# Performance work log

Measured on AMD Instinct MI355X. Metric: run time of the kernel, lower is better.

## Reference

```python
import jax, jax.numpy as jnp
import numpy as np

R, B, N, I, O, NB = 8, 4, 1024, 64, 64, 4
EPS = 1e-7  # keras.backend.epsilon()


def setup_inputs() -> dict:
    key = jax.random.key(0)
    ks = jax.random.split(key, 6)
    features = jax.random.normal(ks[0], (B, N, I), jnp.float32)
    adj = jax.random.randint(ks[1], (R, B, N, N), 0, 2, jnp.int32)  # stacked A[i]
    weight = jax.random.normal(ks[2], (NB, I, O), jnp.float32) * 0.1  # basis weights
    Wo = jax.random.normal(ks[3], (I, O), jnp.float32) * 0.1          # self-loop weight
    w_cmp = jax.random.normal(ks[4], (R, NB), jnp.float32) * 0.1      # basis coefficients
    b = jax.random.normal(ks[5], (O,), jnp.float32) * 0.1             # bias
    return {"features": features, "adj": adj, "weight": weight, "Wo": Wo, "w_cmp": w_cmp, "b": b}


def reference(features, adj, weight, Wo, w_cmp, b):
    # basis decomposition: per-relation weight [R, I, O]
    w_full = jnp.einsum('rb,bio->rio', w_cmp, weight)
    adj_f = adj.astype(features.dtype)                      # [R, B, N, N]
    # per-relation transform: x_r = features @ W_r -> [R, B, N, O]
    x = jnp.einsum('bni,rio->rbno', features, w_full)
    # batch_dot(edges^T, x): agg[r,b,n] = sum_m edges[r,b,m,n] * x[r,b,m]
    agg = jnp.einsum('rbmn,rbmo->rbno', adj_f, x)
    # original normalizer: K.sum(edges, axis=2, keepdims=True) -> row sums over last axis
    deg = adj_f.sum(axis=-1, keepdims=True)                 # [R, B, N, 1]
    agg = agg / (deg + EPS)
    self_x = features @ Wo                                  # [B, N, O]
    # concatenate [x_0 | x_1 | ... | x_{R-1} | self] along features
    concat = jnp.concatenate(
        [agg.transpose(1, 2, 0, 3).reshape(B, N, R * O), self_x], axis=-1
    )                                                       # [B, N, (R+1)*O]
    # faithful to original: reshape (..., O, R+1) then sum last axis
    out = concat.reshape(-1, N, O, R + 1).sum(axis=-1)      # [B, N, O]
    out = out + b
    return jax.nn.relu(out)
```

## Files before the change

### kernel.cpp

```cpp
#include <hip/hip_runtime.h>
#include <hip/hip_bf16.h>


#define NN 1024
#define EPSK 1e-7f

typedef __bf16 bf16x8 __attribute__((ext_vector_type(8)));
typedef float f32x4 __attribute__((ext_vector_type(4)));

__device__ __forceinline__ unsigned short f2bf(float f) {
  union { float f; unsigned int u; } v; v.f = f;
  return (unsigned short)((v.u + 0x7FFFu + ((v.u >> 16) & 1u)) >> 16);
}

__global__ __launch_bounds__(256) void prep_kernel(
    const float* __restrict__ feat,
    const float* __restrict__ weight,
    const float* __restrict__ Wo,
    const float* __restrict__ wcmp,
    float* __restrict__ xf,
    float* __restrict__ selfP,
    float* __restrict__ deg)
{
  __shared__ __align__(16) unsigned short featL[128 * 72];
  __shared__ __align__(16) float wTf[64 * 65];
  __shared__ __align__(16) unsigned short wfold[16 * 72];
  __shared__ __align__(16) float stg[128 * 8];

  const int bid = blockIdx.x;
  const int t = threadIdx.x;
  const bool isSelf = bid >= 256;
  int r, b, chunk;
  if (!isSelf) { r = bid >> 5; b = (bid >> 3) & 3; chunk = bid & 7; }
  else { const int s2 = bid - 256; b = s2 >> 3; chunk = s2 & 7; r = 8; }
  const int n0 = chunk << 7;

  if (bid < 32) {
    for (int k = t; k < NN; k += 256) deg[bid * NN + k] = 0.0f;
  }

  const float* fsrc = feat + ((size_t)(b * NN + n0)) * 64;
  #pragma unroll
  for (int p = 0; p < 8; ++p) {
    const int idx = p * 256 + t;
    const int row = idx >> 4, c4 = idx & 15;
    const float4 v = *reinterpret_cast<const float4*>(fsrc + row * 64 + c4 * 4);
    ushort4 u;
    u.x = f2bf(v.x); u.y = f2bf(v.y); u.z = f2bf(v.z); u.w = f2bf(v.w);
    *reinterpret_cast<ushort4*>(&featL[row * 72 + c4 * 4]) = u;
  }

  if (!isSelf) {
    const float wc0 = wcmp[r * 4 + 0], wc1 = wcmp[r * 4 + 1];
    const float wc2 = wcmp[r * 4 + 2], wc3 = wcmp[r * 4 + 3];
    #pragma unroll
    for (int jj = 0; jj < 16; ++jj) {
      const int e = jj * 256 + t;
      const int i = e >> 6, c = e & 63;
      wTf[c * 65 + i] = wc0 * weight[i * 64 + c] + wc1 * weight[4096 + i * 64 + c] +
                        wc2 * weight[8192 + i * 64 + c] + wc3 * weight[12288 + i * 64 + c];
    }
  } else {
    #pragma unroll
    for (int jj = 0; jj < 16; ++jj) {
      const int e = jj * 256 + t;
      const int i = e >> 6, c = e & 63;
      wTf[c * 65 + i] = Wo[i * 64 + c];
    }
  }
  __syncthreads();

  #pragma unroll
  for (int jj = 0; jj < 4; ++jj) {
    const int e = jj * 256 + t;
    const int s = e >> 6, i = e & 63;
    float sum = 0.f;
    if (s < 8) {
      const int c0 = 9 * s - r;
      const int clo = c0 < 0 ? 0 : c0;
      const int chi = (c0 + 8 > 63) ? 63 : c0 + 8;
      for (int c = clo; c <= chi; ++c) sum += wTf[c * 65 + i];
    }
    wfold[s * 72 + i] = f2bf(sum);
  }
  __syncthreads();

  const int w = t >> 6, lane = t & 63;
  const int li = lane & 15, lg = lane >> 4;

  f32x4 acc0 = {0.f, 0.f, 0.f, 0.f}, acc1 = {0.f, 0.f, 0.f, 0.f};
  #pragma unroll
  for (int ks = 0; ks < 2; ++ks) {
    const int kof = ks * 32 + lg * 8;
    const bf16x8 af = __builtin_bit_cast(bf16x8,
        *reinterpret_cast<const uint4*>(&wfold[li * 72 + kof]));
    const bf16x8 b0 = __builtin_bit_cast(bf16x8,
        *reinterpret_cast<const uint4*>(&featL[((2 * w + 0) * 16 + li) * 72 + kof]));
    const bf16x8 b1 = __builtin_bit_cast(bf16x8,
        *reinterpret_cast<const uint4*>(&featL[((2 * w + 1) * 16 + li) * 72 + kof]));
    acc0 = __builtin_amdgcn_mfma_f32_16x16x32_bf16(af, b0, acc0, 0, 0, 0);
    acc1 = __builtin_amdgcn_mfma_f32_16x16x32_bf16(af, b1, acc1, 0, 0, 0);
  }

  if (lg < 2) {
    #pragma unroll
    for (int qq = 0; qq < 4; ++qq) {
      const int s = lg * 4 + qq;
      stg[((2 * w + 0) * 16 + li) * 8 + s] = acc0[qq];
      stg[((2 * w + 1) * 16 + li) * 8 + s] = acc1[qq];
    }
  }
  __syncthreads();
  {
    float* dstF = isSelf ? (selfP + ((size_t)(b * NN + n0)) * 8)
                         : (xf + ((size_t)((r * 4 + b) * NN + n0)) * 8);
    *reinterpret_cast<float4*>(dstF + t * 4) =
        *reinterpret_cast<const float4*>(&stg[t * 4]);
  }
}

__global__ __launch_bounds__(256) void agg_kernel(
    const int* __restrict__ adj,
    const float* __restrict__ xf,
    float* __restrict__ aggP,
    float* __restrict__ deg)
{
  __shared__ __align__(16) float xsL[256 * 8];
  __shared__ __align__(16) float degL[256 * 66];

  const int bid = blockIdx.x;
  const int rb = bid >> 4, mq = (bid >> 2) & 3, nq = bid & 3;
  const int t = threadIdx.x;
  const int tm = t >> 6, tn = t & 63;
  const int mbase = mq << 8, nbase = nq << 8;

  {
    const float* xs = xf + ((size_t)(rb * NN + mbase)) * 8;
    *reinterpret_cast<float4*>(&xsL[t * 8]) = *reinterpret_cast<const float4*>(xs + t * 8);
    *reinterpret_cast<float4*>(&xsL[t * 8 + 4]) = *reinterpret_cast<const float4*>(xs + t * 8 + 4);
  }

  const int* asrc = adj + (((size_t)rb) << 20) + ((size_t)mbase << 10) + nbase + (tn << 2);

  float acc[4][8];
  #pragma unroll
  for (int j = 0; j < 4; ++j)
    #pragma unroll
    for (int s = 0; s < 8; ++s) acc[j][s] = 0.f;

  __syncthreads();

  int4 buf0 = *reinterpret_cast<const int4*>(asrc + ((size_t)(0 * 4 + tm) << 10));
  int4 buf1 = *reinterpret_cast<const int4*>(asrc + ((size_t)(1 * 4 + tm) << 10));
  int4 buf2 = *reinterpret_cast<const int4*>(asrc + ((size_t)(2 * 4 + tm) << 10));
  int4 buf3 = *reinterpret_cast<const int4*>(asrc + ((size_t)(3 * 4 + tm) << 10));

#define AGG_BODY(BUF, I)                                                        \
  {                                                                             \
    const int4 cur_ = BUF;                                                      \
    const int ml_ = ((I) << 2) + tm;                                            \
    if ((I) < 60) {                                                             \
      BUF = *reinterpret_cast<const int4*>(asrc + ((size_t)(ml_ + 16) << 10));  \
    }                                                                           \
    const float a0_ = (float)cur_.x, a1_ = (float)cur_.y;                       \
    const float a2_ = (float)cur_.z, a3_ = (float)cur_.w;                       \
    degL[ml_ * 66 + tn] = (float)(cur_.x + cur_.y + cur_.z + cur_.w);           \
    const float4 xlo_ = *reinterpret_cast<const float4*>(&xsL[ml_ * 8]);        \
    const float4 xhi_ = *reinterpret_cast<const float4*>(&xsL[ml_ * 8 + 4]);    \
    const float xs_[8] = {xlo_.x, xlo_.y, xlo_.z, xlo_.w,                       \
                          xhi_.x, xhi_.y, xhi_.z, xhi_.w};                      \
    _Pragma("unroll")                                                           \
    for (int s_ = 0; s_ < 8; ++s_) {                                            \
      acc[0][s_] = fmaf(a0_, xs_[s_], acc[0][s_]);                              \
      acc[1][s_] = fmaf(a1_, xs_[s_], acc[1][s_]);                              \
      acc[2][s_] = fmaf(a2_, xs_[s_], acc[2][s_]);                              \
      acc[3][s_] = fmaf(a3_, xs_[s_], acc[3][s_]);                              \
    }                                                                           \
  }

  for (int ib = 0; ib < 16; ++ib) {
    AGG_BODY(buf0, ib * 4 + 0);
    AGG_BODY(buf1, ib * 4 + 1);
    AGG_BODY(buf2, ib * 4 + 2);
    AGG_BODY(buf3, ib * 4 + 3);
  }
#undef AGG_BODY

  __syncthreads();

  {
    float s = 0.f;
    #pragma unroll
    for (int k = 0; k < 32; ++k) {
      const float2 v = *reinterpret_cast<const float2*>(&degL[t * 66 + 2 * k]);
      s += v.x + v.y;
    }
    atomicAdd(&deg[rb * NN + mbase + t], s);
  }
  __syncthreads();

  float* accL = degL;
  #pragma unroll
  for (int j = 0; j < 4; ++j) {
    *reinterpret_cast<float4*>(&accL[t * 36 + j * 8]) =
        make_float4(acc[j][0], acc[j][1], acc[j][2], acc[j][3]);
    *reinterpret_cast<float4*>(&accL[t * 36 + j * 8 + 4]) =
        make_float4(acc[j][4], acc[j][5], acc[j][6], acc[j][7]);
  }
  __syncthreads();
  {
    const int nl = t;
    const int tn2 = nl >> 2, j2 = nl & 3;
    float o8[8];
    #pragma unroll
    for (int s = 0; s < 8; ++s) o8[s] = 0.f;
    #pragma unroll
    for (int tm2 = 0; tm2 < 4; ++tm2) {
      const int base = (tm2 * 64 + tn2) * 36 + j2 * 8;
      const float4 lo = *reinterpret_cast<const float4*>(&accL[base]);
      const float4 hi = *reinterpret_cast<const float4*>(&accL[base + 4]);
      o8[0] += lo.x; o8[1] += lo.y; o8[2] += lo.z; o8[3] += lo.w;
      o8[4] += hi.x; o8[5] += hi.y; o8[6] += hi.z; o8[7] += hi.w;
    }
    float* dst = aggP + (((size_t)(mq * 32 + rb)) * NN + nbase + nl) * 8;
    *reinterpret_cast<float4*>(dst) = make_float4(o8[0], o8[1], o8[2], o8[3]);
    *reinterpret_cast<float4*>(dst + 4) = make_float4(o8[4], o8[5], o8[6], o8[7]);
  }
}

__global__ __launch_bounds__(256) void out_kernel(
    const float* __restrict__ aggP,
    const float* __restrict__ selfP,
    const float* __restrict__ deg,
    const float* __restrict__ bias, float* __restrict__ out)
{
  const int gid = blockIdx.x * 256 + threadIdx.x;
  const int o = gid & 63;
  const int n = (gid >> 6) & 1023;
  const int b = gid >> 16;

  const int r1 = (9 * o) >> 6;
  const int r2 = (9 * o + 8) >> 6;

  float acc = bias[o];
  #pragma unroll
  for (int pass = 0; pass < 2; ++pass) {
    const int r = pass ? r2 : r1;
    if (pass && r2 == r1) break;
    const int s = o - 7 * r;
    float v;
    if (r < 8) {
      const size_t base = (((size_t)(r * 4 + b)) * NN + n) * 8 + s;
      v = aggP[base] + aggP[base + 262144] + aggP[base + 524288] + aggP[base + 786432];
      v /= (deg[(r * 4 + b) * NN + n] + EPSK);
    } else {
      v = selfP[((size_t)(b * NN + n)) * 8 + (o - 56)];
    }
    acc += v;
  }
  out[gid] = fmaxf(acc, 0.0f);
}

extern "C" void kernel_launch(void* const* d_in, const int* in_sizes, int n_in,
                              void* d_out, int out_size, void* d_ws, size_t ws_size,
                              hipStream_t stream) {
  const float* feat   = (const float*)d_in[0];
  const int*   adj    = (const int*)d_in[1];
  const float* weight = (const float*)d_in[2];
  const float* Wo     = (const float*)d_in[3];
  const float* wcmp   = (const float*)d_in[4];
  const float* bias   = (const float*)d_in[5];
  float* out = (float*)d_out;

  char* ws = (char*)d_ws;
  float* xf    = (float*)(ws);
  float* selfP = (float*)(ws + 1048576u);
  float* aggP  = (float*)(ws + 1048576u + 131072u);
  float* deg   = (float*)(ws + 1048576u + 131072u + 4194304u);

  prep_kernel<<<dim3(288), dim3(256), 0, stream>>>(feat, weight, Wo, wcmp, xf, selfP, deg);
  agg_kernel<<<dim3(512), dim3(256), 0, stream>>>(adj, xf, aggP, deg);
  out_kernel<<<dim3(1024), dim3(256), 0, stream>>>(aggP, selfP, deg, bias, out);
}
```

Baseline: 35.24 us.

## Retile aggregation so each block owns full adjacency rows and computes degree directly

The aggregation kernel now gives each block 128 source rows across all 1024 destination columns, so each thread accumulates four columns over all rows without cross-warp reduction. This lets the kernel compute each row's degree completely within one block using byte-packed partial sums in shared memory, which removes the atomicAdd, the deg zeroing in the prep kernel and the shared-memory accumulator reduction. The cost is that partial aggregates are split 8 ways instead of 4, doubling the aggP workspace and the reads in the output kernel. The grid also halves to 256 blocks, each holding 16 int4 prefetches in registers under launch_bounds(256,1).

New measurement: 38.42 us. +9.0%, slower.

```diff
diff --git a/kernel.cpp b/kernel.cpp
--- a/kernel.cpp
+++ b/kernel.cpp
@@ -19,8 +19,7 @@
     const float* __restrict__ Wo,
     const float* __restrict__ wcmp,
     float* __restrict__ xf,
-    float* __restrict__ selfP,
-    float* __restrict__ deg)
+    float* __restrict__ selfP)
 {
   __shared__ __align__(16) unsigned short featL[128 * 72];
   __shared__ __align__(16) float wTf[64 * 65];
@@ -34,10 +33,6 @@
   if (!isSelf) { r = bid >> 5; b = (bid >> 3) & 3; chunk = bid & 7; }
   else { const int s2 = bid - 256; b = s2 >> 3; chunk = s2 & 7; r = 8; }
   const int n0 = chunk << 7;
-
-  if (bid < 32) {
-    for (int k = t; k < NN; k += 256) deg[bid * NN + k] = 0.0f;
-  }
 
   const float* fsrc = feat + ((size_t)(b * NN + n0)) * 64;
   #pragma unroll
@@ -119,112 +114,118 @@
   }
 }
 
-__global__ __launch_bounds__(256) void agg_kernel(
+#define BODY(PK, G, K, PF)                                                      \
+  {                                                                             \
+    const int4 cur_ = PK;                                                       \
+    if (PF) {                                                                   \
+      PK = *reinterpret_cast<const int4*>(asrc + ((((G) << 4) + (K) + 16) << 10)); \
+    }                                                                           \
+    const int ps_ = cur_.x + cur_.y + cur_.z + cur_.w;                          \
+    pk |= ((unsigned int)ps_) << (8 * ((K) & 3));                               \
+    const float a0_ = (float)cur_.x, a1_ = (float)cur_.y;                       \
+    const float a2_ = (float)cur_.z, a3_ = (float)cur_.w;                       \
+    const float4 xlo_ =                                                         \
+        *reinterpret_cast<const float4*>(&xsL[(((G) << 4) + (K)) * 8]);         \
+    const float4 xhi_ =                                                         \
+        *reinterpret_cast<const float4*>(&xsL[(((G) << 4) + (K)) * 8 + 4]);     \
+    const float xv_[8] = {xlo_.x, xlo_.y, xlo_.z, xlo_.w,                       \
+                          xhi_.x, xhi_.y, xhi_.z, xhi_.w};                      \
+    _Pragma("unroll")                                                           \
+    for (int s_ = 0; s_ < 8; ++s_) {                                            \
+      acc0[s_] = fmaf(a0_, xv_[s_], acc0[s_]);                                  \
+      acc1[s_] = fmaf(a1_, xv_[s_], acc1[s_]);                                  \
+      acc2[s_] = fmaf(a2_, xv_[s_], acc2[s_]);                                  \
+      acc3[s_] = fmaf(a3_, xv_[s_], acc3[s_]);                                  \
+    }                                                                           \
+    if (((K) & 3) == 3) {                                                       \
+      degL[((G) * 4 + ((K) >> 2)) * 260 + t] = pk;                              \
+      pk = 0u;                                                                  \
+    }                                                                           \
+  }
+
+#define GROUP(G, PF)                                                            \
+  BODY(P0, G, 0, PF) BODY(P1, G, 1, PF) BODY(P2, G, 2, PF) BODY(P3, G, 3, PF)   \
+  BODY(P4, G, 4, PF) BODY(P5, G, 5, PF) BODY(P6, G, 6, PF) BODY(P7, G, 7, PF)   \
+  BODY(P8, G, 8, PF) BODY(P9, G, 9, PF) BODY(P10, G, 10, PF)                    \
+  BODY(P11, G, 11, PF) BODY(P12, G, 12, PF) BODY(P13, G, 13, PF)                \
+  BODY(P14, G, 14, PF) BODY(P15, G, 15, PF)
+
+__global__ __launch_bounds__(256, 1) void agg_kernel(
     const int* __restrict__ adj,
     const float* __restrict__ xf,
     float* __restrict__ aggP,
     float* __restrict__ deg)
 {
-  __shared__ __align__(16) float xsL[256 * 8];
-  __shared__ __align__(16) float degL[256 * 66];
+  __shared__ __align__(16) float xsL[128 * 8];
+  __shared__ __align__(16) unsigned int degL[32 * 260];
 
   const int bid = blockIdx.x;
-  const int rb = bid >> 4, mq = (bid >> 2) & 3, nq = bid & 3;
+  const int rb = bid >> 3, mc = bid & 7;
+  const int m0 = mc << 7;
   const int t = threadIdx.x;
-  const int tm = t >> 6, tn = t & 63;
-  const int mbase = mq << 8, nbase = nq << 8;
+
+  const int* asrc = adj + (((size_t)rb) << 20) + (((size_t)m0) << 10) + (t << 2);
+
+  int4 P0  = *reinterpret_cast<const int4*>(asrc + (0 << 10));
+  int4 P1  = *reinterpret_cast<const int4*>(asrc + (1 << 10));
+  int4 P2  = *reinterpret_cast<const int4*>(asrc + (2 << 10));
+  int4 P3  = *reinterpret_cast<const int4*>(asrc + (3 << 10));
+  int4 P4  = *reinterpret_cast<const int4*>(asrc + (4 << 10));
+  int4 P5  = *reinterpret_cast<const int4*>(asrc + (5 << 10));
+  int4 P6  = *reinterpret_cast<const int4*>(asrc + (6 << 10));
+  int4 P7  = *reinterpret_cast<const int4*>(asrc + (7 << 10));
+  int4 P8  = *reinterpret_cast<const int4*>(asrc + (8 << 10));
+  int4 P9  = *reinterpret_cast<const int4*>(asrc + (9 << 10));
+  int4 P10 = *reinterpret_cast<const int4*>(asrc + (10 << 10));
+  int4 P11 = *reinterpret_cast<const int4*>(asrc + (11 << 10));
+  int4 P12 = *reinterpret_cast<const int4*>(asrc + (12 << 10));
+  int4 P13 = *reinterpret_cast<const int4*>(asrc + (13 << 10));
+  int4 P14 = *reinterpret_cast<const int4*>(asrc + (14 << 10));
+  int4 P15 = *reinterpret_cast<const int4*>(asrc + (15 << 10));
 
   {
-    const float* xs = xf + ((size_t)(rb * NN + mbase)) * 8;
-    *reinterpret_cast<float4*>(&xsL[t * 8]) = *reinterpret_cast<const float4*>(xs + t * 8);
-    *reinterpret_cast<float4*>(&xsL[t * 8 + 4]) = *reinterpret_cast<const float4*>(xs + t * 8 + 4);
-  }
-
-  const int* asrc = adj + (((size_t)rb) << 20) + ((size_t)mbase << 10) + nbase + (tn << 2);
-
-  float acc[4][8];
-  #pragma unroll
-  for (int j = 0; j < 4; ++j)
-    #pragma unroll
-    for (int s = 0; s < 8; ++s) acc[j][s] = 0.f;
-
-  __syncthreads();
-
-  int4 buf0 = *reinterpret_cast<const int4*>(asrc + ((size_t)(0 * 4 + tm) << 10));
-  int4 buf1 = *reinterpret_cast<const int4*>(asrc + ((size_t)(1 * 4 + tm) << 10));
-  int4 buf2 = *reinterpret_cast<const int4*>(asrc + ((size_t)(2 * 4 + tm) << 10));
-  int4 buf3 = *reinterpret_cast<const int4*>(asrc + ((size_t)(3 * 4 + tm) << 10));
-
-#define AGG_BODY(BUF, I)                                                        \
-  {                                                                             \
-    const int4 cur_ = BUF;                                                      \
-    const int ml_ = ((I) << 2) + tm;                                            \
-    if ((I) < 60) {                                                             \
-      BUF = *reinterpret_cast<const int4*>(asrc + ((size_t)(ml_ + 16) << 10));  \
-    }                                                                           \
-    const float a0_ = (float)cur_.x, a1_ = (float)cur_.y;                       \
-    const float a2_ = (float)cur_.z, a3_ = (float)cur_.w;                       \
-    degL[ml_ * 66 + tn] = (float)(cur_.x + cur_.y + cur_.z + cur_.w);           \
-    const float4 xlo_ = *reinterpret_cast<const float4*>(&xsL[ml_ * 8]);        \
-    const float4 xhi_ = *reinterpret_cast<const float4*>(&xsL[ml_ * 8 + 4]);    \
-    const float xs_[8] = {xlo_.x, xlo_.y, xlo_.z, xlo_.w,                       \
-                          xhi_.x, xhi_.y, xhi_.z, xhi_.w};                      \
-    _Pragma("unroll")                                                           \
-    for (int s_ = 0; s_ < 8; ++s_) {                                            \
-      acc[0][s_] = fmaf(a0_, xs_[s_], acc[0][s_]);                              \
-      acc[1][s_] = fmaf(a1_, xs_[s_], acc[1][s_]);                              \
-      acc[2][s_] = fmaf(a2_, xs_[s_], acc[2][s_]);                              \
-      acc[3][s_] = fmaf(a3_, xs_[s_], acc[3][s_]);                              \
-    }                                                                           \
-  }
-
-  for (int ib = 0; ib < 16; ++ib) {
-    AGG_BODY(buf0, ib * 4 + 0);
-    AGG_BODY(buf1, ib * 4 + 1);
-    AGG_BODY(buf2, ib * 4 + 2);
-    AGG_BODY(buf3, ib * 4 + 3);
-  }
-#undef AGG_BODY
-
-  __syncthreads();
+    const float* xs = xf + ((size_t)(rb * NN + m0)) * 8;
+    *reinterpret_cast<float4*>(&xsL[t * 4]) =
+        *reinterpret_cast<const float4*>(xs + t * 4);
+  }
+
+  float acc0[8], acc1[8], acc2[8], acc3[8];
+  #pragma unroll
+  for (int s = 0; s < 8; ++s) { acc0[s] = 0.f; acc1[s] = 0.f; acc2[s] = 0.f; acc3[s] = 0.f; }
+
+  __syncthreads();
+
+  unsigned int pk = 0u;
+  for (int g = 0; g < 7; ++g) {
+    GROUP(g, 1)
+  }
+  GROUP(7, 0)
 
   {
-    float s = 0.f;
-    #pragma unroll
-    for (int k = 0; k < 32; ++k) {
-      const float2 v = *reinterpret_cast<const float2*>(&degL[t * 66 + 2 * k]);
-      s += v.x + v.y;
-    }
-    atomicAdd(&deg[rb * NN + mbase + t], s);
-  }
-  __syncthreads();
-
-  float* accL = degL;
-  #pragma unroll
-  for (int j = 0; j < 4; ++j) {
-    *reinterpret_cast<float4*>(&accL[t * 36 + j * 8]) =
-        make_float4(acc[j][0], acc[j][1], acc[j][2], acc[j][3]);
-    *reinterpret_cast<float4*>(&accL[t * 36 + j * 8 + 4]) =
-        make_float4(acc[j][4], acc[j][5], acc[j][6], acc[j][7]);
-  }
-  __syncthreads();
-  {
-    const int nl = t;
-    const int tn2 = nl >> 2, j2 = nl & 3;
-    float o8[8];
-    #pragma unroll
-    for (int s = 0; s < 8; ++s) o8[s] = 0.f;
-    #pragma unroll
-    for (int tm2 = 0; tm2 < 4; ++tm2) {
-      const int base = (tm2 * 64 + tn2) * 36 + j2 * 8;
-      const float4 lo = *reinterpret_cast<const float4*>(&accL[base]);
-      const float4 hi = *reinterpret_cast<const float4*>(&accL[base + 4]);
-      o8[0] += lo.x; o8[1] += lo.y; o8[2] += lo.z; o8[3] += lo.w;
-      o8[4] += hi.x; o8[5] += hi.y; o8[6] += hi.z; o8[7] += hi.w;
-    }
-    float* dst = aggP + (((size_t)(mq * 32 + rb)) * NN + nbase + nl) * 8;
-    *reinterpret_cast<float4*>(dst) = make_float4(o8[0], o8[1], o8[2], o8[3]);
-    *reinterpret_cast<float4*>(dst + 4) = make_float4(o8[4], o8[5], o8[6], o8[7]);
+    float* dst = aggP + (((size_t)(mc * 32 + rb)) * NN + 4 * (size_t)t) * 8;
+    *reinterpret_cast<float4*>(dst + 0)  = make_float4(acc0[0], acc0[1], acc0[2], acc0[3]);
+    *reinterpret_cast<float4*>(dst + 4)  = make_float4(acc0[4], acc0[5], acc0[6], acc0[7]);
+    *reinterpret_cast<float4*>(dst + 8)  = make_float4(acc1[0], acc1[1], acc1[2], acc1[3]);
+    *reinterpret_cast<float4*>(dst + 12) = make_float4(acc1[4], acc1[5], acc1[6], acc1[7]);
+    *reinterpret_cast<float4*>(dst + 16) = make_float4(acc2[0], acc2[1], acc2[2], acc2[3]);
+    *reinterpret_cast<float4*>(dst + 20) = make_float4(acc2[4], acc2[5], acc2[6], acc2[7]);
+    *reinterpret_cast<float4*>(dst + 24) = make_float4(acc3[0], acc3[1], acc3[2], acc3[3]);
+    *reinterpret_cast<float4*>(dst + 28) = make_float4(acc3[4], acc3[5], acc3[6], acc3[7]);
+  }
+
+  __syncthreads();
+
+  if (t < 128) {
+    const unsigned int* src = &degL[(t >> 2) * 260];
+    const int sh = 8 * (t & 3);
+    int sum = 0;
+    #pragma unroll
+    for (int c4 = 0; c4 < 64; ++c4) {
+      const uint4 v = *reinterpret_cast<const uint4*>(src + c4 * 4);
+      sum += (int)((v.x >> sh) & 0xFFu) + (int)((v.y >> sh) & 0xFFu) +
+             (int)((v.z >> sh) & 0xFFu) + (int)((v.w >> sh) & 0xFFu);
+    }
+    deg[rb * NN + m0 + t] = (float)sum;
   }
 }
 
@@ -247,12 +248,14 @@
   for (int pass = 0; pass < 2; ++pass) {
     const int r = pass ? r2 : r1;
     if (pass && r2 == r1) break;
-    const int s = o - 7 * r;
     float v;
     if (r < 8) {
+      const int s = o - 7 * r;
       const size_t base = (((size_t)(r * 4 + b)) * NN + n) * 8 + s;
-      v = aggP[base] + aggP[base + 262144] + aggP[base + 524288] + aggP[base + 786432];
-      v /= (deg[(r * 4 + b) * NN + n] + EPSK);
+      float sum = 0.f;
+      #pragma unroll
+      for (int c = 0; c < 8; ++c) sum += aggP[base + (size_t)c * 262144];
+      v = sum / (deg[(r * 4 + b) * NN + n] + EPSK);
     } else {
       v = selfP[((size_t)(b * NN + n)) * 8 + (o - 56)];
     }
@@ -276,9 +279,9 @@
   float* xf    = (float*)(ws);
   float* selfP = (float*)(ws + 1048576u);
   float* aggP  = (float*)(ws + 1048576u + 131072u);
-  float* deg   = (float*)(ws + 1048576u + 131072u + 4194304u);
-
-  prep_kernel<<<dim3(288), dim3(256), 0, stream>>>(feat, weight, Wo, wcmp, xf, selfP, deg);
-  agg_kernel<<<dim3(512), dim3(256), 0, stream>>>(adj, xf, aggP, deg);
+  float* deg   = (float*)(ws + 1048576u + 131072u + 8388608u);
+
+  prep_kernel<<<dim3(288), dim3(256), 0, stream>>>(feat, weight, Wo, wcmp, xf, selfP);
+  agg_kernel<<<dim3(256), dim3(256), 0, stream>>>(adj, xf, aggP, deg);
   out_kernel<<<dim3(1024), dim3(256), 0, stream>>>(aggP, selfP, deg, bias, out);
 }
```
